# Kernel optimization log

Measured on AMD Instinct MI355X. Metric: run time of the kernel, lower is better.

Reference implementation:

```python
import jax, jax.numpy as jnp
import numpy as np

B, S, D_IN, D_INT, D_OUT, E, K_SYN = 2, 2048, 2048, 2048, 2048, 4, 512
GROUPS = D_INT // 8  # Conv1d groups

def setup_inputs() -> dict:
    key = jax.random.key(0)
    ks = jax.random.split(key, 20)
    n = lambda k, sh, std: jax.random.normal(k, sh, dtype=jnp.float32) * std
    d = {}
    d['x'] = jax.random.normal(ks[0], (B, S, D_IN), dtype=jnp.float32)
    d['syntax_ids'] = jax.random.randint(ks[1], (B, S), 0, K_SYN, dtype=jnp.int32)
    d['W_in'] = n(ks[2], (D_IN, D_INT), D_IN ** -0.5)
    d['b_in'] = jnp.zeros((D_INT,), jnp.float32)
    d['W_syn_emb'] = n(ks[3], (K_SYN, D_INT // 4), 0.02)
    d['W_syn'] = n(ks[4], (D_INT + D_INT // 4, D_INT), 0.02)
    d['b_syn'] = jnp.zeros((D_INT,), jnp.float32)
    d['W_gate'] = n(ks[5], (D_INT, 1), 0.02)
    d['b_gate'] = jnp.zeros((1,), jnp.float32)
    d['W_router'] = n(ks[6], (D_INT, E), 0.02)
    d['b_router'] = jnp.zeros((E,), jnp.float32)
    d['W_e1'] = n(ks[7], (E, D_INT, 2 * D_INT), 0.02)
    d['b_e1'] = jnp.zeros((E, 2 * D_INT), jnp.float32)
    d['W_e2'] = n(ks[8], (E, 2 * D_INT, D_INT), 0.02)
    d['b_e2'] = jnp.zeros((E, D_INT), jnp.float32)
    d['W_ctx'] = n(ks[9], (D_INT, D_INT), D_INT ** -0.5)
    d['b_ctx'] = jnp.zeros((D_INT,), jnp.float32)
    fan = 8 * 3 + 8 * 3
    lim = float(np.sqrt(6.0 / fan))
    d['conv_w'] = jax.random.uniform(ks[10], (D_INT, 8, 3), jnp.float32, -lim, lim)
    d['conv_b'] = jnp.zeros((D_INT,), jnp.float32)
    d['W_out'] = n(ks[11], (D_INT, D_OUT), D_INT ** -0.5)
    d['b_out'] = jnp.zeros((D_OUT,), jnp.float32)
    return d

def _forward(x, syntax_ids, W_in, b_in, W_syn_emb, W_syn, b_syn, W_gate, b_gate,
             W_router, b_router, W_e1, b_e1, W_e2, b_e2, W_ctx, b_ctx,
             conv_w, conv_b, W_out, b_out):
    # input projection + SiLU (dropout is identity in eval / p=0)
    h = jax.nn.silu(jnp.einsum('bsi,id->bsd', x, W_in) + b_in)
    # syntax-aware projection
    se = W_syn_emb[syntax_ids]                       # [B,S,D/4] gather
    h = jnp.einsum('bsc,cd->bsd', jnp.concatenate([h, se], axis=-1), W_syn) + b_syn
    # adaptive computation gate
    gate = jax.nn.sigmoid(jnp.einsum('bsd,do->bso', h, W_gate) + b_gate)
    h = h * gate
    # dense mixture-of-experts combine (softmax router weights)
    probs = jax.nn.softmax(jnp.einsum('bsd,de->bse', h, W_router) + b_router, axis=-1)
    eh = jax.nn.silu(jnp.einsum('bsd,edf->bsef', h, W_e1) + b_e1)   # [B,S,E,2D]
    eo = jnp.einsum('bsef,efd->bsed', eh, W_e2) + b_e2              # [B,S,E,D]
    h = h + jnp.einsum('bsed,bse->bsd', eo, probs)
    # code-specific: context linear + grouped Conv1d pattern extractor
    ctx = jnp.einsum('bsd,df->bsf', h, W_ctx) + b_ctx
    hc = jnp.transpose(h, (0, 2, 1))  # [B,D,S]
    pat = jax.lax.conv_general_dilated(
        hc, conv_w, window_strides=(1,), padding=((1, 1),),
        dimension_numbers=('NCH', 'OIH', 'NCH'), feature_group_count=GROUPS)
    pat = jnp.transpose(pat + conv_b[None, :, None], (0, 2, 1))
    h = h + ctx + pat
    out = jnp.einsum('bsd,do->bso', h, W_out) + b_out
    return out + x  # residual (input_dim == output_dim)

def reference(x, syntax_ids, W_in, b_in, W_syn_emb, W_syn, b_syn, W_gate, b_gate,
              W_router, b_router, W_e1, b_e1, W_e2, b_e2, W_ctx, b_ctx,
              conv_w, conv_b, W_out, b_out):
    return _forward(x, syntax_ids, W_in, b_in, W_syn_emb, W_syn, b_syn, W_gate,
                    b_gate, W_router, b_router, W_e1, b_e1, W_e2, b_e2,
                    W_ctx, b_ctx, conv_w, conv_b, W_out, b_out)
```

## Files before the change

### kernel.cpp

```cpp
#include <hip/hip_runtime.h>

typedef __attribute__((ext_vector_type(8))) short short8;
typedef __attribute__((ext_vector_type(4))) float floatx4;

__device__ __forceinline__ float b2f(ushort us) {
    union { unsigned u; float f; } v; v.u = ((unsigned)us) << 16; return v.f;
}
__device__ __forceinline__ ushort f2b(float f) {
    union { float f; unsigned u; } v; v.f = f;
    unsigned r = (v.u + 0x7fffu + ((v.u >> 16) & 1u)) >> 16;
    return (ushort)r;
}
__device__ __forceinline__ float ldany(const void* p, long i, int bf) {
    return bf ? b2f(((const ushort*)p)[i]) : ((const float*)p)[i];
}
__device__ __forceinline__ void async16(const ushort* g, ushort* l) {
    __builtin_amdgcn_global_load_lds((const __attribute__((address_space(1))) void*)g,
                                     (__attribute__((address_space(3))) void*)l,
                                     16, 0, 0);
}

__global__ void detect_dtype(const unsigned* __restrict__ w, int* __restrict__ flag)
{
    if (threadIdx.x == 0 && blockIdx.x == 0) {
        int votes = 0;
        for (int i = 0; i < 256; i++) {
            unsigned e = (w[i] >> 7) & 0xFFu;
            if (e >= 112u && e <= 128u) votes++;
        }
        *flag = (votes >= 128) ? 1 : 0;
    }
}

__global__ __launch_bounds__(256) void transpose_any(
    const void* __restrict__ in, long in_off, ushort* __restrict__ out,
    int R, int C, const int* __restrict__ flag)
{
    __shared__ float tile[64][65];
    const int bf = *flag;
    const int t  = threadIdx.x;
    const long r0 = (long)blockIdx.y * 64;
    const long c0 = (long)blockIdx.x * 64;
    const int rl = t >> 4;
    const int cl = (t & 15) * 4;
    #pragma unroll
    for (int p = 0; p < 4; p++) {
        const int r = rl + p * 16;
        const long base = in_off + (r0 + r) * C + c0 + cl;
        if (bf) {
            ushort4 v = *(const ushort4*)((const ushort*)in + base);
            tile[r][cl + 0] = b2f(v.x); tile[r][cl + 1] = b2f(v.y);
            tile[r][cl + 2] = b2f(v.z); tile[r][cl + 3] = b2f(v.w);
        } else {
            float4 v = *(const float4*)((const float*)in + base);
            tile[r][cl + 0] = v.x; tile[r][cl + 1] = v.y;
            tile[r][cl + 2] = v.z; tile[r][cl + 3] = v.w;
        }
    }
    __syncthreads();
    #pragma unroll
    for (int p = 0; p < 4; p++) {
        const int oc = rl + p * 16;
        ushort4 v;
        v.x = f2b(tile[cl + 0][oc]); v.y = f2b(tile[cl + 1][oc]);
        v.z = f2b(tile[cl + 2][oc]); v.w = f2b(tile[cl + 3][oc]);
        *(ushort4*)(out + (c0 + oc) * R + r0 + cl) = v;
    }
}

__global__ void to_bf16_any(const void* __restrict__ in, ushort* __restrict__ out,
                            long n4, const int* __restrict__ flag)
{
    const long i = (long)blockIdx.x * blockDim.x + threadIdx.x;
    if (i >= n4) return;
    const int bf = *flag;
    ushort4 o;
    if (bf) {
        o = ((const ushort4*)in)[i];
    } else {
        float4 v = ((const float4*)in)[i];
        o.x = f2b(v.x); o.y = f2b(v.y); o.z = f2b(v.z); o.w = f2b(v.w);
    }
    ((ushort4*)out)[i] = o;
}

__global__ void f32_to_bf16_4(const float* __restrict__ in, ushort* __restrict__ out, long n4)
{
    const long i = (long)blockIdx.x * blockDim.x + threadIdx.x;
    if (i >= n4) return;
    float4 v = ((const float4*)in)[i];
    ushort4 o; o.x = f2b(v.x); o.y = f2b(v.y); o.z = f2b(v.z); o.w = f2b(v.w);
    ((ushort4*)out)[i] = o;
}

#define EPI_SILU    0
#define EPI_BIAS    1
#define EPI_OUT     2
#define EPI_ATOM    3

#define BAR()        __builtin_amdgcn_s_barrier()
#define WAIT_LGKM0() asm volatile("s_waitcnt lgkmcnt(0)" ::: "memory")
#define WAIT_VM6()   asm volatile("s_waitcnt vmcnt(6)" ::: "memory")
#define WAIT_VM5()   asm volatile("s_waitcnt vmcnt(5)" ::: "memory")
#define WAIT_VM0()   asm volatile("s_waitcnt vmcnt(0)" ::: "memory")

#define STAGE_A(BUF, H, KT) do {                                               \
    const long _k0 = zoff + ((long)(KT) << 6);                                 \
    _Pragma("unroll")                                                          \
    for (int _i = 0; _i < AINSTR; ++_i) {                                      \
        const int _gi   = w + _i * 8;                                          \
        const int _s    = _gi / AHALF_GRP;                                     \
        const int _wg   = _gi % AHALF_GRP;                                     \
        const int _row0 = _s * (BM / 2) + (H) * (BM / 4) + _wg * 8;            \
        const int _grow = _row0 + (lane >> 3);                                 \
        async16(A + (m0 + _grow) * (long)lda + _k0 +                           \
                    (((lane & 7) ^ (_grow & 7)) << 3),                         \
                smem + (BUF) * BUFU + _row0 * 64);                             \
    } } while (0)

#define STAGE_B(BUF, H, KT) do {                                               \
    const long _k0 = zoff + ((long)(KT) << 6);                                 \
    _Pragma("unroll")                                                          \
    for (int _i = 0; _i < 2; ++_i) {                                           \
        const int _gi   = w * 2 + _i;                                          \
        const int _row0 = (_gi >> 2) * 64 + (H) * 32 + (_gi & 3) * 8;          \
        const int _grow = _row0 + (lane >> 3);                                 \
        async16(Bt + (n0 + _grow) * (long)lda + _k0 +                          \
                     (((lane & 7) ^ (_grow & 7)) << 3),                        \
                smem + (BUF) * BUFU + BM * 64 + _row0 * 64);                   \
    } } while (0)

#define LOAD_A(BUF, MH) do {                                                   \
    _Pragma("unroll")                                                          \
    for (int _m = 0; _m < MF / 2; ++_m) {                                      \
        const int _row = wm * (BM / 2) + ((MH) * (MF / 2) + _m) * 16 + fr;     \
        _Pragma("unroll")                                                      \
        for (int _ks = 0; _ks < 2; ++_ks)                                      \
            a[_m][_ks] = *(const short8*)(smem + (BUF) * BUFU + _row * 64 +    \
                                          (((_ks * 4 + q) ^ (_row & 7)) << 3));\
    } } while (0)

#define LOAD_B(BUF, NH, BREG) do {                                             \
    _Pragma("unroll")                                                          \
    for (int _n = 0; _n < 2; ++_n) {                                           \
        const int _row = wn * 64 + ((NH) * 2 + _n) * 16 + fr;                  \
        _Pragma("unroll")                                                      \
        for (int _ks = 0; _ks < 2; ++_ks)                                      \
            BREG[_n][_ks] = *(const short8*)(smem + (BUF) * BUFU + BM * 64 +   \
                                             _row * 64 +                       \
                                          (((_ks * 4 + q) ^ (_row & 7)) << 3));\
    } } while (0)

#define MMA(MH, NH, BREG) do {                                                 \
    _Pragma("unroll")                                                          \
    for (int _m = 0; _m < MF / 2; ++_m)                                        \
    _Pragma("unroll")                                                          \
    for (int _n = 0; _n < 2; ++_n)                                             \
    _Pragma("unroll")                                                          \
    for (int _ks = 0; _ks < 2; ++_ks)                                          \
        acc[(MH) * (MF / 2) + _m][(NH) * 2 + _n] =                             \
            __builtin_amdgcn_mfma_f32_16x16x32_bf16(                           \
                a[_m][_ks], BREG[_n][_ks],                                     \
                acc[(MH) * (MF / 2) + _m][(NH) * 2 + _n], 0, 0, 0);            \
    } while (0)

template<int EPI, int MF>
__global__ __launch_bounds__(512, 2) void gemm8(
    const ushort* __restrict__ A, const ushort* __restrict__ Bt,
    int M, int N, int lda, int kslice,
    const void* __restrict__ bias, long bias_off,
    void* __restrict__ out, long ldo,
    float* __restrict__ hacc,
    const float* __restrict__ rowscale,
    const ushort* __restrict__ resid,
    const int* __restrict__ flag)
{
    constexpr int BM        = MF * 32;
    constexpr int AHALF_GRP = BM / 32;
    constexpr int AINSTR    = BM / 128;
    constexpr int BUFU      = (BM + 256) * 64;
    extern __shared__ ushort smem[];

    const int tid  = threadIdx.x;
    const int lane = tid & 63;
    const int w    = tid >> 6;
    const int wm   = w >> 2;
    const int wn   = w & 3;
    const int fr   = lane & 15;
    const int q    = lane >> 4;
    const long m0  = (long)blockIdx.y * BM;
    const long n0  = (long)blockIdx.x * 256;
    const long zoff = (long)blockIdx.z * kslice;
    const int NT   = kslice >> 6;

    floatx4 acc[MF][4] = {};
    short8 a[MF / 2][2];
    short8 b0[2][2], b1[2][2];

    STAGE_A(0, 0, 0); STAGE_A(0, 1, 0); STAGE_B(0, 0, 0); STAGE_B(0, 1, 0);
    STAGE_A(1, 0, 1); STAGE_B(1, 0, 1); STAGE_B(1, 1, 1);
    if constexpr (MF == 8) WAIT_VM6(); else WAIT_VM5();
    BAR();

    for (int t = 0; t < NT; ++t) {
        const int cur = t & 1, nxt = cur ^ 1;
        LOAD_A(cur, 0);
        LOAD_B(cur, 0, b0);
        if (t + 1 < NT) STAGE_A(nxt, 1, t + 1);
        BAR(); WAIT_LGKM0();
        __builtin_amdgcn_s_setprio(1); MMA(0, 0, b0); __builtin_amdgcn_s_setprio(0);
        BAR();
        LOAD_B(cur, 1, b1);
        if (t + 2 < NT) STAGE_A(cur, 0, t + 2);
        BAR(); WAIT_LGKM0();
        __builtin_amdgcn_s_setprio(1); MMA(0, 1, b1); __builtin_amdgcn_s_setprio(0);
        BAR();
        LOAD_A(cur, 1);
        if (t + 2 < NT) STAGE_B(cur, 0, t + 2);
        BAR(); WAIT_LGKM0();
        __builtin_amdgcn_s_setprio(1); MMA(1, 1, b1); __builtin_amdgcn_s_setprio(0);
        BAR();
        if (t + 2 < NT) {
            STAGE_B(cur, 1, t + 2);
            if constexpr (MF == 8) WAIT_VM6(); else WAIT_VM5();
        } else {
            WAIT_VM0();
        }
        BAR();
        __builtin_amdgcn_s_setprio(1); MMA(1, 0, b0); __builtin_amdgcn_s_setprio(0);
        BAR();
    }

    const int bf = *flag;
    const bool addb = (EPI != EPI_ATOM) || (blockIdx.z == 0);
    #pragma unroll
    for (int i = 0; i < MF; ++i) {
        #pragma unroll
        for (int r = 0; r < 4; ++r) {
            const long m = m0 + wm * (BM / 2) + i * 16 + q * 4 + r;
            #pragma unroll
            for (int j = 0; j < 4; ++j) {
                const long n = n0 + wn * 64 + j * 16 + fr;
                float v = acc[i][j][r] + (addb ? ldany(bias, bias_off + n, bf) : 0.f);
                if (EPI == EPI_SILU) {
                    v = v / (1.f + __expf(-v));
                    ((ushort*)out)[m * ldo + n] = f2b(v);
                } else if (EPI == EPI_BIAS) {
                    ((ushort*)out)[m * ldo + n] = f2b(v);
                } else if (EPI == EPI_ATOM) {
                    atomicAdd(&hacc[m * (long)N + n],
                              rowscale ? rowscale[m * 4] * v : v);
                } else {
                    v += b2f(resid[m * (long)N + n]);
                    if (bf) ((ushort*)out)[m * ldo + n] = f2b(v);
                    else    ((float*)out)[m * ldo + n]  = v;
                }
            }
        }
    }
}

__global__ void gather_syn(const int* __restrict__ ids, const void* __restrict__ emb,
                           ushort* __restrict__ hA, const int* __restrict__ flag)
{
    const int bf = *flag;
    const long m = blockIdx.x;
    const int id = ids[m];
    const int j = threadIdx.x * 2;
    float a, b;
    if (bf) {
        ushort2 v = *(const ushort2*)((const ushort*)emb + (long)id * 512 + j);
        a = b2f(v.x); b = b2f(v.y);
    } else {
        float2 v = *(const float2*)((const float*)emb + (long)id * 512 + j);
        a = v.x; b = v.y;
    }
    ushort2 o; o.x = f2b(a); o.y = f2b(b);
    *(ushort2*)(hA + m * 2560 + 2048 + j) = o;
}

__global__ __launch_bounds__(256) void gate_router(
    ushort* __restrict__ h2, float* __restrict__ hacc, float* __restrict__ probs,
    const void* __restrict__ Wg, const void* __restrict__ bg,
    const void* __restrict__ Wr, const void* __restrict__ br,
    const int* __restrict__ flag)
{
    const int bf = *flag;
    const long m = blockIdx.x;
    const int t = threadIdx.x;
    const int lane = t & 63;
    const int wv = t >> 6;
    ushort* row = h2 + m * 2048;

    float sg = 0.f, s0 = 0.f, s1 = 0.f, s2 = 0.f, s3 = 0.f;
    for (int k = t; k < 2048; k += 256) {
        const float h = b2f(row[k]);
        sg += h * ldany(Wg, k, bf);
        float r0v, r1v, r2v, r3v;
        if (bf) {
            ushort4 v = *(const ushort4*)((const ushort*)Wr + (long)k * 4);
            r0v = b2f(v.x); r1v = b2f(v.y); r2v = b2f(v.z); r3v = b2f(v.w);
        } else {
            float4 v = *(const float4*)((const float*)Wr + (long)k * 4);
            r0v = v.x; r1v = v.y; r2v = v.z; r3v = v.w;
        }
        s0 += h * r0v; s1 += h * r1v; s2 += h * r2v; s3 += h * r3v;
    }
    #pragma unroll
    for (int off = 32; off > 0; off >>= 1) {
        sg += __shfl_down(sg, off);
        s0 += __shfl_down(s0, off);
        s1 += __shfl_down(s1, off);
        s2 += __shfl_down(s2, off);
        s3 += __shfl_down(s3, off);
    }
    __shared__ float red[4][5];
    __shared__ float gate_bc;
    if (lane == 0) {
        red[wv][0] = sg; red[wv][1] = s0; red[wv][2] = s1;
        red[wv][3] = s2; red[wv][4] = s3;
    }
    __syncthreads();
    if (t == 0) {
        float G = red[0][0] + red[1][0] + red[2][0] + red[3][0];
        float R[4];
        #pragma unroll
        for (int e = 0; e < 4; e++)
            R[e] = red[0][1 + e] + red[1][1 + e] + red[2][1 + e] + red[3][1 + e];
        const float gate = 1.f / (1.f + __expf(-(G + ldany(bg, 0, bf))));
        float lg[4], mx = -1e30f;
        #pragma unroll
        for (int e = 0; e < 4; e++) {
            lg[e] = gate * R[e] + ldany(br, e, bf);
            mx = fmaxf(mx, lg[e]);
        }
        float p[4], s = 0.f;
        #pragma unroll
        for (int e = 0; e < 4; e++) { p[e] = __expf(lg[e] - mx); s += p[e]; }
        #pragma unroll
        for (int e = 0; e < 4; e++) probs[m * 4 + e] = p[e] / s;
        gate_bc = gate;
    }
    __syncthreads();
    const float gate = gate_bc;
    for (int k = t; k < 2048; k += 256) {
        const float v = b2f(row[k]) * gate;
        row[k] = f2b(v);
        hacc[m * 2048 + k] = v;
    }
}

__global__ __launch_bounds__(256) void conv_combine(
    const ushort* __restrict__ h4, const float* __restrict__ hacc,
    const void* __restrict__ cw, const void* __restrict__ cb,
    ushort* __restrict__ h5, const int* __restrict__ flag)
{
    const int S = 2048, D = 2048;
    const int SC = 32;
    const int bf = *flag;
    const int b  = blockIdx.z;
    const int c0 = blockIdx.y * 512;
    const int s0 = blockIdx.x * SC;
    const int t  = threadIdx.x;

    __shared__ ushort tile[(SC + 2) * 512];

    const int cp = 2 * t;
    const int c  = c0 + cp;
    float w0[3][8], w1[3][8];
    #pragma unroll
    for (int kk = 0; kk < 3; kk++)
        #pragma unroll
        for (int ii = 0; ii < 8; ii++) {
            w0[kk][ii] = ldany(cw, (long)c * 24 + ii * 3 + kk, bf);
            w1[kk][ii] = ldany(cw, (long)(c + 1) * 24 + ii * 3 + kk, bf);
        }
    const float bc0 = ldany(cb, c, bf);
    const float bc1 = ldany(cb, c + 1, bf);

    for (int idx = t; idx < (SC + 2) * 64; idx += 256) {
        const int r  = idx >> 6;
        const int ch = (idx & 63) * 8;
        const int s  = s0 - 1 + r;
        short8 v = {};
        if (s >= 0 && s < S)
            v = *(const short8*)(h4 + ((long)b * S + s) * D + c0 + ch);
        *(short8*)(tile + r * 512 + ch) = v;
    }
    __syncthreads();

    const int gc8 = (cp >> 3) * 8;
    for (int sl = 0; sl < SC; ++sl) {
        float p0 = 0.f, p1 = 0.f;
        #pragma unroll
        for (int kk = 0; kk < 3; kk++) {
            short8 v = *(const short8*)(tile + (sl + kk) * 512 + gc8);
            #pragma unroll
            for (int ii = 0; ii < 8; ii++) {
                const float x = b2f((ushort)v[ii]);
                p0 += x * w0[kk][ii];
                p1 += x * w1[kk][ii];
            }
        }
        const long m = (long)b * S + s0 + sl;
        const float2 ha = *(const float2*)(hacc + m * D + c);
        ushort2 o; o.x = f2b(ha.x + bc0 + p0); o.y = f2b(ha.y + bc1 + p1);
        *(ushort2*)(h5 + m * D + c) = o;
    }
}

extern "C" void kernel_launch(void* const* d_in, const int* in_sizes, int n_in,
                              void* d_out, int out_size, void* d_ws, size_t ws_size,
                              hipStream_t stream)
{
    (void)in_sizes; (void)n_in; (void)out_size; (void)ws_size;
    const void* x        = d_in[0];
    const int*  syn      = (const int*)d_in[1];
    const void* W_in     = d_in[2];
    const void* b_in     = d_in[3];
    const void* W_synemb = d_in[4];
    const void* W_syn    = d_in[5];
    const void* b_syn    = d_in[6];
    const void* W_gate   = d_in[7];
    const void* b_gate   = d_in[8];
    const void* W_router = d_in[9];
    const void* b_router = d_in[10];
    const void* W_e1     = d_in[11];
    const void* b_e1     = d_in[12];
    const void* W_e2     = d_in[13];
    const void* b_e2     = d_in[14];
    const void* W_ctx    = d_in[15];
    const void* b_ctx    = d_in[16];
    const void* conv_w   = d_in[17];
    const void* conv_b   = d_in[18];
    const void* W_out    = d_in[19];
    const void* b_out    = d_in[20];

    char* ws = (char*)d_ws;
    int*    flag  = (int*)ws;
    ushort* WT    = (ushort*)(ws + 256);
    ushort* xb    = (ushort*)(ws + 16777472);
    ushort* hA    = (ushort*)(ws + 33554688);
    ushort* eh    = (ushort*)(ws + 16777472);
    ushort* h23   = (ushort*)(ws + 54526208);
    float*  probs = (float*)(ws + 71303424);
    float*  hacc  = (float*)(ws + 71368960);
    const int M = 4096;
    dim3 blk(256);
    const int LDS4 = 98304;
    const int LDS8 = 131072;

    static bool attr_set = false;
    if (!attr_set) {
        (void)hipFuncSetAttribute(reinterpret_cast<const void*>(&gemm8<EPI_SILU, 4>),
                                  hipFuncAttributeMaxDynamicSharedMemorySize, LDS4);
        (void)hipFuncSetAttribute(reinterpret_cast<const void*>(&gemm8<EPI_BIAS, 4>),
                                  hipFuncAttributeMaxDynamicSharedMemorySize, LDS4);
        (void)hipFuncSetAttribute(reinterpret_cast<const void*>(&gemm8<EPI_OUT,  4>),
                                  hipFuncAttributeMaxDynamicSharedMemorySize, LDS4);
        (void)hipFuncSetAttribute(reinterpret_cast<const void*>(&gemm8<EPI_SILU, 8>),
                                  hipFuncAttributeMaxDynamicSharedMemorySize, LDS8);
        (void)hipFuncSetAttribute(reinterpret_cast<const void*>(&gemm8<EPI_ATOM, 8>),
                                  hipFuncAttributeMaxDynamicSharedMemorySize, LDS8);
        attr_set = true;
    }

    detect_dtype<<<dim3(1), dim3(64), 0, stream>>>((const unsigned*)W_in, flag);
    to_bf16_any<<<dim3(8192), blk, 0, stream>>>(x, xb, 2097152L, flag);

    transpose_any<<<dim3(32, 32), blk, 0, stream>>>(W_in, 0, WT, 2048, 2048, flag);
    gemm8<EPI_SILU, 4><<<dim3(8, 32), dim3(512), LDS4, stream>>>(
        xb, WT, M, 2048, 2048, 2048, b_in, 0, hA, 2560, nullptr, nullptr, nullptr, flag);
    gather_syn<<<dim3(4096), blk, 0, stream>>>(syn, W_synemb, hA, flag);
    transpose_any<<<dim3(32, 40), blk, 0, stream>>>(W_syn, 0, WT, 2560, 2048, flag);
    gemm8<EPI_BIAS, 4><<<dim3(8, 32), dim3(512), LDS4, stream>>>(
        hA, WT, M, 2048, 2560, 2560, b_syn, 0, h23, 2048, nullptr, nullptr, nullptr, flag);
    gate_router<<<dim3(4096), blk, 0, stream>>>(
        h23, hacc, probs, W_gate, b_gate, W_router, b_router, flag);
    for (int e = 0; e < 4; e++) {
        transpose_any<<<dim3(64, 32), blk, 0, stream>>>(
            W_e1, (long)e * 8388608, WT, 2048, 4096, flag);
        gemm8<EPI_SILU, 8><<<dim3(16, 16), dim3(512), LDS8, stream>>>(
            h23, WT, M, 4096, 2048, 2048, b_e1, (long)e * 4096, eh, 4096,
            nullptr, nullptr, nullptr, flag);
        transpose_any<<<dim3(32, 64), blk, 0, stream>>>(
            W_e2, (long)e * 8388608, WT, 4096, 2048, flag);
        gemm8<EPI_ATOM, 8><<<dim3(8, 16, 2), dim3(512), LDS8, stream>>>(
            eh, WT, M, 2048, 4096, 2048, b_e2, (long)e * 2048, nullptr, 0,
            hacc, probs + e, nullptr, flag);
    }
    to_bf16_any<<<dim3(8192), blk, 0, stream>>>(x, xb, 2097152L, flag);
    f32_to_bf16_4<<<dim3(8192), blk, 0, stream>>>(hacc, h23, 2097152L);
    transpose_any<<<dim3(32, 32), blk, 0, stream>>>(W_ctx, 0, WT, 2048, 2048, flag);
    gemm8<EPI_ATOM, 8><<<dim3(8, 16, 2), dim3(512), LDS8, stream>>>(
        h23, WT, M, 2048, 2048, 1024, b_ctx, 0, nullptr, 0,
        hacc, nullptr, nullptr, flag);
    conv_combine<<<dim3(64, 4, 2), blk, 0, stream>>>(
        h23, hacc, conv_w, conv_b, hA, flag);
    transpose_any<<<dim3(32, 32), blk, 0, stream>>>(W_out, 0, WT, 2048, 2048, flag);
    gemm8<EPI_OUT, 4><<<dim3(8, 32), dim3(512), LDS4, stream>>>(
        hA, WT, M, 2048, 2048, 2048, b_out, 0, d_out, 2048, nullptr, nullptr, xb, flag);
}
```

Measured before the change: 1.607 ms.

## Replace split-K atomics with per-slice partial buffers and a fused reduction

Split-K GEMMs for the expert down-projection and the context projection stop using float atomicAdd. When the workspace is large enough, each K-slice writes or accumulates into its own fp32 partial buffer, and a new reduce_snap kernel (or conv_combine) sums the partials. When the workspace is too small, a non-split BM=128 GEMM does a plain read-modify-write into hacc. The residual now reads x directly, so the second x-to-bf16 conversion is dropped. The cost is extra fp32 partial traffic and workspace use, plus a fallback path with lower parallelism.

```diff
diff --git a/kernel.cpp b/kernel.cpp
--- a/kernel.cpp
+++ b/kernel.cpp
@@ -93,10 +93,28 @@
     ((ushort4*)out)[i] = o;
 }
 
+__global__ __launch_bounds__(256) void reduce_snap(
+    float* __restrict__ hacc, const float* __restrict__ p0,
+    const float* __restrict__ p1, ushort* __restrict__ h4o, long n4)
+{
+    const long i = (long)blockIdx.x * blockDim.x + threadIdx.x;
+    if (i >= n4) return;
+    float4 a = ((const float4*)hacc)[i];
+    const float4 b = ((const float4*)p0)[i];
+    const float4 c = ((const float4*)p1)[i];
+    a.x += b.x + c.x; a.y += b.y + c.y; a.z += b.z + c.z; a.w += b.w + c.w;
+    ((float4*)hacc)[i] = a;
+    ushort4 o; o.x = f2b(a.x); o.y = f2b(a.y); o.z = f2b(a.z); o.w = f2b(a.w);
+    ((ushort4*)h4o)[i] = o;
+}
+
 #define EPI_SILU    0
 #define EPI_BIAS    1
 #define EPI_OUT     2
-#define EPI_ATOM    3
+#define EPI_EXPERT  3
+#define EPI_CTX     4
+#define EPI_PARTI   5
+#define EPI_PARTA   6
 
 #define BAR()        __builtin_amdgcn_s_barrier()
 #define WAIT_LGKM0() asm volatile("s_waitcnt lgkmcnt(0)" ::: "memory")
@@ -172,7 +190,7 @@
     void* __restrict__ out, long ldo,
     float* __restrict__ hacc,
     const float* __restrict__ rowscale,
-    const ushort* __restrict__ resid,
+    const void* __restrict__ resid,
     const int* __restrict__ flag)
 {
     constexpr int BM        = MF * 32;
@@ -232,7 +250,7 @@
     }
 
     const int bf = *flag;
-    const bool addb = (EPI != EPI_ATOM) || (blockIdx.z == 0);
+    const bool addb = (EPI != EPI_PARTI && EPI != EPI_PARTA) || (blockIdx.z == 0);
     #pragma unroll
     for (int i = 0; i < MF; ++i) {
         #pragma unroll
@@ -247,11 +265,18 @@
                     ((ushort*)out)[m * ldo + n] = f2b(v);
                 } else if (EPI == EPI_BIAS) {
                     ((ushort*)out)[m * ldo + n] = f2b(v);
-                } else if (EPI == EPI_ATOM) {
-                    atomicAdd(&hacc[m * (long)N + n],
-                              rowscale ? rowscale[m * 4] * v : v);
+                } else if (EPI == EPI_EXPERT) {
+                    hacc[m * (long)N + n] += rowscale[m * 4] * v;
+                } else if (EPI == EPI_CTX) {
+                    hacc[m * (long)N + n] += v;
+                } else if (EPI == EPI_PARTI || EPI == EPI_PARTA) {
+                    float* pz = hacc + (long)blockIdx.z * (long)M * N;
+                    const float sv = rowscale ? rowscale[m * 4] * v : v;
+                    const long idx = m * (long)N + n;
+                    if (EPI == EPI_PARTI) pz[idx] = sv;
+                    else                  pz[idx] += sv;
                 } else {
-                    v += b2f(resid[m * (long)N + n]);
+                    v += ldany(resid, m * (long)N + n, bf);
                     if (bf) ((ushort*)out)[m * ldo + n] = f2b(v);
                     else    ((float*)out)[m * ldo + n]  = v;
                 }
@@ -352,6 +377,7 @@
 
 __global__ __launch_bounds__(256) void conv_combine(
     const ushort* __restrict__ h4, const float* __restrict__ hacc,
+    const float* __restrict__ p0, const float* __restrict__ p1,
     const void* __restrict__ cw, const void* __restrict__ cb,
     ushort* __restrict__ h5, const int* __restrict__ flag)
 {
@@ -391,20 +417,25 @@
 
     const int gc8 = (cp >> 3) * 8;
     for (int sl = 0; sl < SC; ++sl) {
-        float p0 = 0.f, p1 = 0.f;
+        float pa0 = 0.f, pa1 = 0.f;
         #pragma unroll
         for (int kk = 0; kk < 3; kk++) {
             short8 v = *(const short8*)(tile + (sl + kk) * 512 + gc8);
             #pragma unroll
             for (int ii = 0; ii < 8; ii++) {
                 const float x = b2f((ushort)v[ii]);
-                p0 += x * w0[kk][ii];
-                p1 += x * w1[kk][ii];
+                pa0 += x * w0[kk][ii];
+                pa1 += x * w1[kk][ii];
             }
         }
         const long m = (long)b * S + s0 + sl;
-        const float2 ha = *(const float2*)(hacc + m * D + c);
-        ushort2 o; o.x = f2b(ha.x + bc0 + p0); o.y = f2b(ha.y + bc1 + p1);
+        float2 ha = *(const float2*)(hacc + m * D + c);
+        if (p0) {
+            const float2 e0 = *(const float2*)(p0 + m * D + c);
+            const float2 e1 = *(const float2*)(p1 + m * D + c);
+            ha.x += e0.x + e1.x; ha.y += e0.y + e1.y;
+        }
+        ushort2 o; o.x = f2b(ha.x + bc0 + pa0); o.y = f2b(ha.y + bc1 + pa1);
         *(ushort2*)(h5 + m * D + c) = o;
     }
 }
@@ -413,7 +444,7 @@
                               void* d_out, int out_size, void* d_ws, size_t ws_size,
                               hipStream_t stream)
 {
-    (void)in_sizes; (void)n_in; (void)out_size; (void)ws_size;
+    (void)in_sizes; (void)n_in; (void)out_size;
     const void* x        = d_in[0];
     const int*  syn      = (const int*)d_in[1];
     const void* W_in     = d_in[2];
@@ -445,6 +476,9 @@
     ushort* h23   = (ushort*)(ws + 54526208);
     float*  probs = (float*)(ws + 71303424);
     float*  hacc  = (float*)(ws + 71368960);
+    float*  part0 = (float*)(ws + 104923392UL);
+    float*  part1 = (float*)(ws + 138477824UL);
+    const bool use_split = ws_size >= 172032256UL;
     const int M = 4096;
     dim3 blk(256);
     const int LDS4 = 98304;
@@ -452,15 +486,21 @@
 
     static bool attr_set = false;
     if (!attr_set) {
-        (void)hipFuncSetAttribute(reinterpret_cast<const void*>(&gemm8<EPI_SILU, 4>),
+        (void)hipFuncSetAttribute(reinterpret_cast<const void*>(&gemm8<EPI_SILU,   4>),
                                   hipFuncAttributeMaxDynamicSharedMemorySize, LDS4);
-        (void)hipFuncSetAttribute(reinterpret_cast<const void*>(&gemm8<EPI_BIAS, 4>),
+        (void)hipFuncSetAttribute(reinterpret_cast<const void*>(&gemm8<EPI_BIAS,   4>),
                                   hipFuncAttributeMaxDynamicSharedMemorySize, LDS4);
-        (void)hipFuncSetAttribute(reinterpret_cast<const void*>(&gemm8<EPI_OUT,  4>),
+        (void)hipFuncSetAttribute(reinterpret_cast<const void*>(&gemm8<EPI_OUT,    4>),
                                   hipFuncAttributeMaxDynamicSharedMemorySize, LDS4);
-        (void)hipFuncSetAttribute(reinterpret_cast<const void*>(&gemm8<EPI_SILU, 8>),
+        (void)hipFuncSetAttribute(reinterpret_cast<const void*>(&gemm8<EPI_EXPERT, 4>),
+                                  hipFuncAttributeMaxDynamicSharedMemorySize, LDS4);
+        (void)hipFuncSetAttribute(reinterpret_cast<const void*>(&gemm8<EPI_CTX,    4>),
+                                  hipFuncAttributeMaxDynamicSharedMemorySize, LDS4);
+        (void)hipFuncSetAttribute(reinterpret_cast<const void*>(&gemm8<EPI_SILU,   8>),
                                   hipFuncAttributeMaxDynamicSharedMemorySize, LDS8);
-        (void)hipFuncSetAttribute(reinterpret_cast<const void*>(&gemm8<EPI_ATOM, 8>),
+        (void)hipFuncSetAttribute(reinterpret_cast<const void*>(&gemm8<EPI_PARTI,  8>),
+                                  hipFuncAttributeMaxDynamicSharedMemorySize, LDS8);
+        (void)hipFuncSetAttribute(reinterpret_cast<const void*>(&gemm8<EPI_PARTA,  8>),
                                   hipFuncAttributeMaxDynamicSharedMemorySize, LDS8);
         attr_set = true;
     }
@@ -485,19 +525,38 @@
             nullptr, nullptr, nullptr, flag);
         transpose_any<<<dim3(32, 64), blk, 0, stream>>>(
             W_e2, (long)e * 8388608, WT, 4096, 2048, flag);
-        gemm8<EPI_ATOM, 8><<<dim3(8, 16, 2), dim3(512), LDS8, stream>>>(
-            eh, WT, M, 2048, 4096, 2048, b_e2, (long)e * 2048, nullptr, 0,
-            hacc, probs + e, nullptr, flag);
-    }
-    to_bf16_any<<<dim3(8192), blk, 0, stream>>>(x, xb, 2097152L, flag);
-    f32_to_bf16_4<<<dim3(8192), blk, 0, stream>>>(hacc, h23, 2097152L);
+        if (use_split) {
+            if (e == 0)
+                gemm8<EPI_PARTI, 8><<<dim3(8, 16, 2), dim3(512), LDS8, stream>>>(
+                    eh, WT, M, 2048, 4096, 2048, b_e2, (long)e * 2048, nullptr, 0,
+                    part0, probs + e, nullptr, flag);
+            else
+                gemm8<EPI_PARTA, 8><<<dim3(8, 16, 2), dim3(512), LDS8, stream>>>(
+                    eh, WT, M, 2048, 4096, 2048, b_e2, (long)e * 2048, nullptr, 0,
+                    part0, probs + e, nullptr, flag);
+        } else {
+            gemm8<EPI_EXPERT, 4><<<dim3(8, 32), dim3(512), LDS4, stream>>>(
+                eh, WT, M, 2048, 4096, 4096, b_e2, (long)e * 2048, nullptr, 0,
+                hacc, probs + e, nullptr, flag);
+        }
+    }
+    if (use_split)
+        reduce_snap<<<dim3(8192), blk, 0, stream>>>(hacc, part0, part1, h23, 2097152L);
+    else
+        f32_to_bf16_4<<<dim3(8192), blk, 0, stream>>>(hacc, h23, 2097152L);
     transpose_any<<<dim3(32, 32), blk, 0, stream>>>(W_ctx, 0, WT, 2048, 2048, flag);
-    gemm8<EPI_ATOM, 8><<<dim3(8, 16, 2), dim3(512), LDS8, stream>>>(
-        h23, WT, M, 2048, 2048, 1024, b_ctx, 0, nullptr, 0,
-        hacc, nullptr, nullptr, flag);
+    if (use_split)
+        gemm8<EPI_PARTI, 8><<<dim3(8, 16, 2), dim3(512), LDS8, stream>>>(
+            h23, WT, M, 2048, 2048, 1024, b_ctx, 0, nullptr, 0,
+            part0, nullptr, nullptr, flag);
+    else
+        gemm8<EPI_CTX, 4><<<dim3(8, 32), dim3(512), LDS4, stream>>>(
+            h23, WT, M, 2048, 2048, 2048, b_ctx, 0, nullptr, 0,
+            hacc, nullptr, nullptr, flag);
     conv_combine<<<dim3(64, 4, 2), blk, 0, stream>>>(
-        h23, hacc, conv_w, conv_b, hA, flag);
+        h23, hacc, use_split ? part0 : nullptr, use_split ? part1 : nullptr,
+        conv_w, conv_b, hA, flag);
     transpose_any<<<dim3(32, 32), blk, 0, stream>>>(W_out, 0, WT, 2048, 2048, flag);
     gemm8<EPI_OUT, 4><<<dim3(8, 32), dim3(512), LDS4, stream>>>(
-        hA, WT, M, 2048, 2048, 2048, b_out, 0, d_out, 2048, nullptr, nullptr, xb, flag);
-}
+        hA, WT, M, 2048, 2048, 2048, b_out, 0, d_out, 2048, nullptr, nullptr, x, flag);
+}
```

New measurement: 1.579 ms. No clear change (-1.7%).
